# Performance work log

Measured on AMD Instinct MI355X. Metric: run time of the kernel, lower is better.

The kernel has to match this reference:

```python
import jax, jax.numpy as jnp
import numpy as np

B, N, FEAT = 64, 4096, 256
DIM, KVQ, HEADS, SLOTS, ITERS = 256, 256, 4, 8, 3
DPH = KVQ // HEADS
SCALE = DPH ** -0.5
EPS = 1e-8
LN_EPS = 1e-5


def layer_norm(x, w, b):
    mu = x.mean(-1, keepdims=True)
    var = ((x - mu) ** 2).mean(-1, keepdims=True)
    return (x - mu) * jax.lax.rsqrt(var + LN_EPS) * w + b


def setup_inputs() -> dict:
    key = jax.random.key(0)
    ks = jax.random.split(key, 12)
    s = 0.02
    return {
        "inputs": jax.random.normal(ks[0], (B, N, FEAT), jnp.float32),
        "conditioning": jax.random.normal(ks[1], (B, SLOTS, DIM), jnp.float32),
        "ln_in_w": jnp.ones((FEAT,), jnp.float32),
        "ln_in_b": jnp.zeros((FEAT,), jnp.float32),
        "ln_slot_w": jnp.ones((DIM,), jnp.float32),
        "ln_slot_b": jnp.zeros((DIM,), jnp.float32),
        "Wq": jax.random.normal(ks[2], (KVQ, DIM), jnp.float32) * s,
        "Wk": jax.random.normal(ks[3], (KVQ, FEAT), jnp.float32) * s,
        "Wv": jax.random.normal(ks[4], (KVQ, FEAT), jnp.float32) * s,
        "gru_wih": jax.random.normal(ks[5], (3 * DIM, KVQ), jnp.float32) * s,
        "gru_whh": jax.random.normal(ks[6], (3 * DIM, DIM), jnp.float32) * s,
        "gru_bih": jnp.zeros((3 * DIM,), jnp.float32),
        "gru_bhh": jnp.zeros((3 * DIM,), jnp.float32),
    }


def _gru_cell(x, h, wih, whh, bih, bhh):
    # torch.nn.GRUCell semantics; x:[M,KVQ], h:[M,DIM]
    gx = x @ wih.T + bih  # [M, 3*DIM]
    gh = h @ whh.T + bhh
    xr, xz, xn = jnp.split(gx, 3, axis=-1)
    hr, hz, hn = jnp.split(gh, 3, axis=-1)
    r = jax.nn.sigmoid(xr + hr)
    z = jax.nn.sigmoid(xz + hz)
    n = jnp.tanh(xn + r * hn)
    return (1.0 - z) * n + z * h


def reference(inputs, conditioning, ln_in_w, ln_in_b, ln_slot_w, ln_slot_b,
              Wq, Wk, Wv, gru_wih, gru_whh, gru_bih, gru_bhh):
    b, n, _ = inputs.shape
    x = layer_norm(inputs, ln_in_w, ln_in_b)
    k = (x @ Wk.T).reshape(b, n, HEADS, DPH)
    v = (x @ Wv.T).reshape(b, n, HEADS, DPH)

    slots = conditioning
    attn_list = []
    for _ in range(ITERS):
        slots_prev = slots
        sn = layer_norm(slots, ln_slot_w, ln_slot_b)
        q = (sn @ Wq.T).reshape(b, SLOTS, HEADS, DPH) * SCALE
        dots = jnp.einsum('bihd,bjhd->bihj', q, k)  # [b, SLOTS, HEADS, n]
        # softmax over flattened (slots, heads) axis per input position j
        attn = jax.nn.softmax(dots.reshape(b, SLOTS * HEADS, n), axis=1)
        attn = attn.reshape(b, SLOTS, HEADS, n)
        attn_before = attn
        attn = attn / (attn.sum(-1, keepdims=True) + EPS)
        updates = jnp.einsum('bjhd,bihj->bihd', v, attn).reshape(b, SLOTS, KVQ)
        h = _gru_cell(updates.reshape(-1, KVQ), slots_prev.reshape(-1, DIM),
                      gru_wih, gru_whh, gru_bih, gru_bhh)
        slots = h.reshape(b, SLOTS, DIM)
        attn_list.append(attn_before.mean(axis=2))  # [b, SLOTS, n]

    return slots, attn_list[-1], jnp.stack(attn_list)
```

## Files before the change

kernel.cpp:

```cpp
#include <hip/hip_runtime.h>
#include <hip/hip_bf16.h>


typedef unsigned int u32;
typedef unsigned short u16;
typedef short bf16x8 __attribute__((ext_vector_type(8)));
typedef float f32x4 __attribute__((ext_vector_type(4)));

#define SCALE_ 0.125f

__device__ inline u16 f2bf(float f){
  u32 x = __float_as_uint(f);
  return (u16)((x + 0x7fffu + ((x >> 16) & 1u)) >> 16);
}
__device__ inline float bf2f_s(short h){ return __uint_as_float(((u32)(u16)h) << 16); }

__device__ inline void gload16(const void* g, void* l){
  __builtin_amdgcn_global_load_lds((const __attribute__((address_space(1))) u32*)g,
                                   (__attribute__((address_space(3))) u32*)l, 16, 0, 0);
}

__global__ void prep_kernel(const float* __restrict__ Wk, const float* __restrict__ Wv,
                            const float* __restrict__ wih, const float* __restrict__ whh,
                            u16* __restrict__ Bkv, u16* __restrict__ wihb, u16* __restrict__ whhb){
  int t = blockIdx.x * 256 + threadIdx.x;
  int stride = gridDim.x * 256;
  for (int idx = t; idx < 512 * 256; idx += stride){
    int n = idx >> 8, c = idx & 255;
    float v = (n < 256) ? Wk[(n << 8) + c] : Wv[((n - 256) << 8) + c];
    Bkv[idx] = f2bf(v);
  }
  for (int idx = t; idx < 768 * 256; idx += stride){
    wihb[idx] = f2bf(wih[idx]);
    whhb[idx] = f2bf(whh[idx]);
  }
}

__global__ __launch_bounds__(256) void ln_in_kernel(const float* __restrict__ x,
    const float* __restrict__ w, const float* __restrict__ bb, u16* __restrict__ xn){
  int wid = threadIdx.x >> 6, lane = threadIdx.x & 63;
  long row = (long)blockIdx.x * 4 + wid;
  const float4* xr = (const float4*)(x + row * 256);
  float4 v = xr[lane];
  float s  = v.x + v.y + v.z + v.w;
  float s2 = v.x*v.x + v.y*v.y + v.z*v.z + v.w*v.w;
  #pragma unroll
  for (int m = 1; m < 64; m <<= 1){ s += __shfl_xor(s, m); s2 += __shfl_xor(s2, m); }
  float mu = s * (1.f/256.f);
  float rstd = rsqrtf(s2 * (1.f/256.f) - mu*mu + 1e-5f);
  float4 wv = ((const float4*)w)[lane];
  float4 bv = ((const float4*)bb)[lane];
  ushort4 o;
  o.x = f2bf((v.x - mu) * rstd * wv.x + bv.x);
  o.y = f2bf((v.y - mu) * rstd * wv.y + bv.y);
  o.z = f2bf((v.z - mu) * rstd * wv.z + bv.z);
  o.w = f2bf((v.w - mu) * rstd * wv.w + bv.w);
  *(ushort4*)(xn + row * 256 + lane * 4) = o;
}

__global__ __launch_bounds__(256) void gemm_kv(const u16* __restrict__ A,
                                               const u16* __restrict__ Bm,
                                               u16* __restrict__ kv){
  __shared__ u16 smem[16384];
  u16* Al = smem;
  u16* Bl = smem + 8192;
  int tid = threadIdx.x, wid = tid >> 6, lane = tid & 63;
  int nt = blockIdx.x & 3;
  long mt = blockIdx.x >> 2;
  long m0 = mt * 128;
  int n0 = nt * 128;
  f32x4 acc[4][4] = {};
  int msub = (wid & 1) * 64, nsub = (wid >> 1) * 64;
  for (int kt = 0; kt < 4; ++kt){
    const char* Ag = (const char*)(A + m0 * 256 + kt * 64);
    const char* Bg = (const char*)(Bm + (long)n0 * 256 + kt * 64);
    #pragma unroll
    for (int p = 0; p < 4; ++p){
      int r0 = wid * 32 + p * 8;
      gload16(Ag + (long)(r0 + (lane >> 3)) * 512 + (lane & 7) * 16, (char*)Al + r0 * 128);
      gload16(Bg + (long)(r0 + (lane >> 3)) * 512 + (lane & 7) * 16, (char*)Bl + r0 * 128);
    }
    __syncthreads();
    #pragma unroll
    for (int kk = 0; kk < 2; ++kk){
      bf16x8 af[4], bfr[4];
      #pragma unroll
      for (int mi = 0; mi < 4; ++mi)
        af[mi] = *(const bf16x8*)(Al + (msub + mi*16 + (lane & 15)) * 64 + kk * 32 + (lane >> 4) * 8);
      #pragma unroll
      for (int ni = 0; ni < 4; ++ni)
        bfr[ni] = *(const bf16x8*)(Bl + (nsub + ni*16 + (lane & 15)) * 64 + kk * 32 + (lane >> 4) * 8);
      #pragma unroll
      for (int mi = 0; mi < 4; ++mi)
        #pragma unroll
        for (int ni = 0; ni < 4; ++ni)
          acc[mi][ni] = __builtin_amdgcn_mfma_f32_16x16x32_bf16(af[mi], bfr[ni], acc[mi][ni], 0, 0, 0);
    }
    __syncthreads();
  }
  u16* Ct = smem;
  #pragma unroll
  for (int mi = 0; mi < 4; ++mi){
    #pragma unroll
    for (int ni = 0; ni < 4; ++ni){
      int col = nsub + ni*16 + (lane & 15);
      #pragma unroll
      for (int r = 0; r < 4; ++r){
        int rowm = msub + mi*16 + (lane >> 4) * 4 + r;
        Ct[rowm * 128 + col] = f2bf(acc[mi][ni][r]);
      }
    }
  }
  __syncthreads();
  #pragma unroll
  for (int p = 0; p < 8; ++p){
    int g = p * 256 + tid;
    int row = g >> 4, pw = g & 15;
    long m = m0 + row;
    int j = (int)(m & 4095);
    int lloc = pw ^ (j & 7);
    uint4 val = *(const uint4*)(Ct + row * 128 + lloc * 8);
    *(uint4*)((char*)kv + m * 1024 + n0 * 2 + pw * 16) = val;
  }
}

__global__ __launch_bounds__(256) void q_kernel(const float* __restrict__ ssrc,
    const float* __restrict__ lnw, const float* __restrict__ lnb,
    const float* __restrict__ Wq, float* __restrict__ qout){
  __shared__ float sn[256];
  __shared__ float red[8];
  int row = blockIdx.x, t = threadIdx.x;
  int wid = t >> 6, lane = t & 63;
  float x = ssrc[row * 256 + t];
  float s = x, s2 = x * x;
  #pragma unroll
  for (int m = 1; m < 64; m <<= 1){ s += __shfl_xor(s, m); s2 += __shfl_xor(s2, m); }
  if (lane == 0){ red[wid] = s; red[4 + wid] = s2; }
  __syncthreads();
  s  = red[0] + red[1] + red[2] + red[3];
  s2 = red[4] + red[5] + red[6] + red[7];
  float mu = s * (1.f/256.f);
  float rstd = rsqrtf(s2 * (1.f/256.f) - mu*mu + 1e-5f);
  sn[t] = (x - mu) * rstd * lnw[t] + lnb[t];
  __syncthreads();
  const float4* wr = (const float4*)(Wq + t * 256);
  float acc = 0.f;
  #pragma unroll 8
  for (int c = 0; c < 64; ++c){
    float4 wv = wr[c];
    acc += wv.x * sn[c*4] + wv.y * sn[c*4+1] + wv.z * sn[c*4+2] + wv.w * sn[c*4+3];
  }
  qout[row * 256 + t] = acc * SCALE_;
}

__global__ __launch_bounds__(256) void iter_kernel(
    const u16* __restrict__ kv, const float* __restrict__ qg,
    float* __restrict__ upd, float* __restrict__ asum,
    float* __restrict__ out_stack, float* __restrict__ out_last, int write_last){
  __shared__ u16 kvl[32 * 512];
  __shared__ float ql[2048];
  __shared__ float expl[1024];
  __shared__ float rtot[32];
  int tid = threadIdx.x, wid = tid >> 6, lane = tid & 63;
  int b = blockIdx.x >> 4;
  int blk = blockIdx.x & 15;

  {
    const char* qsrc = (const char*)(qg + b * 2048);
    #pragma unroll
    for (int p = 0; p < 2; ++p){
      int seg = wid * 2 + p;
      gload16(qsrc + seg * 1024 + lane * 16, (char*)ql + seg * 1024);
    }
  }
  float updacc[8];
  #pragma unroll
  for (int e = 0; e < 8; ++e) updacc[e] = 0.f;
  float asacc = 0.f;
  int i_u = tid >> 5, h_u = (tid >> 3) & 3, c_u = tid & 7;
  int jj = lane & 31, half = lane >> 5, h = wid;

  for (int tile = 0; tile < 8; ++tile){
    int j0 = (blk * 8 + tile) * 32;
    const char* src = (const char*)(kv + ((long)b * 4096 + j0) * 512);
    #pragma unroll
    for (int p = 0; p < 8; ++p){
      int seg = wid * 8 + p;
      gload16(src + seg * 1024 + lane * 16, (char*)kvl + seg * 1024);
    }
    __syncthreads();
    float dots[8];
    #pragma unroll
    for (int i = 0; i < 8; ++i) dots[i] = 0.f;
    #pragma unroll
    for (int cc = 0; cc < 4; ++cc){
      int c = half * 4 + cc;
      int gq = jj * 64 + ((h * 8 + c) ^ (jj & 7));
      bf16x8 kvv = *(const bf16x8*)(kvl + gq * 8);
      float kf[8];
      #pragma unroll
      for (int e = 0; e < 8; ++e) kf[e] = bf2f_s(kvv[e]);
      #pragma unroll
      for (int i = 0; i < 8; ++i){
        const float4* q4 = (const float4*)(ql + ((i * 4 + h) << 6) + c * 8);
        float4 qa = q4[0], qb = q4[1];
        dots[i] += qa.x*kf[0] + qa.y*kf[1] + qa.z*kf[2] + qa.w*kf[3]
                 + qb.x*kf[4] + qb.y*kf[5] + qb.z*kf[6] + qb.w*kf[7];
      }
    }
    #pragma unroll
    for (int i = 0; i < 8; ++i) dots[i] += __shfl_xor(dots[i], 32);
    float ev[8];
    #pragma unroll
    for (int i = 0; i < 8; ++i) ev[i] = __expf(dots[i]);
    #pragma unroll
    for (int r = 0; r < 4; ++r){
      int i = half * 4 + r;
      expl[jj * 32 + ((h * 8 + i) ^ jj)] = ev[i];
    }
    __syncthreads();
    if (wid == 0 && lane < 32){
      int j = lane;
      float tot = 0.f; float si[8];
      #pragma unroll
      for (int i = 0; i < 8; ++i) si[i] = 0.f;
      #pragma unroll
      for (int h2 = 0; h2 < 4; ++h2){
        #pragma unroll
        for (int i = 0; i < 8; ++i){
          float v = expl[j * 32 + ((h2 * 8 + i) ^ j)];
          tot += v; si[i] += v;
        }
      }
      float rt = 1.f / tot;
      rtot[j] = rt;
      long obase = ((long)b * 8) * 4096 + j0 + j;
      #pragma unroll
      for (int i = 0; i < 8; ++i){
        float o = 0.25f * si[i] * rt;
        out_stack[obase + (long)i * 4096] = o;
        if (write_last) out_last[obase + (long)i * 4096] = o;
      }
    }
    __syncthreads();
    #pragma unroll 4
    for (int j = 0; j < 32; ++j){
      float at = expl[j * 32 + ((h_u * 8 + i_u) ^ j)] * rtot[j];
      int gv = j * 64 + ((32 + h_u * 8 + c_u) ^ (j & 7));
      bf16x8 vv = *(const bf16x8*)(kvl + gv * 8);
      #pragma unroll
      for (int e = 0; e < 8; ++e) updacc[e] += at * bf2f_s(vv[e]);
      if (c_u == 0) asacc += at;
    }
    __syncthreads();
  }
  float* up = upd + (((long)b * 8 + i_u) << 8) + h_u * 64 + c_u * 8;
  #pragma unroll
  for (int e = 0; e < 8; ++e) atomicAdd(up + e, updacc[e]);
  if (c_u == 0) atomicAdd(asum + ((b * 8 + i_u) << 2) + h_u, asacc);
}

__global__ __launch_bounds__(256) void gru_kernel(const float* __restrict__ upd,
    const float* __restrict__ asum, const float* __restrict__ hsrc,
    const u16* __restrict__ wihb, const u16* __restrict__ whhb,
    const float* __restrict__ bih, const float* __restrict__ bhh,
    float* __restrict__ slots_ws, float* __restrict__ out_slots, int write_out){
  __shared__ float xs[256], hs[256];
  int row = blockIdx.x, t = threadIdx.x;
  float a = asum[(row << 2) + (t >> 6)];
  xs[t] = upd[(row << 8) + t] / (a + 1e-8f);
  hs[t] = hsrc[(row << 8) + t];
  __syncthreads();
  float gx[3], gh[3];
  #pragma unroll
  for (int g = 0; g < 3; ++g){
    const bf16x8* wr = (const bf16x8*)(wihb + (g * 256 + t) * 256);
    const bf16x8* wh = (const bf16x8*)(whhb + (g * 256 + t) * 256);
    float ax = 0.f, ah = 0.f;
    for (int c = 0; c < 32; ++c){
      bf16x8 w1 = wr[c], w2 = wh[c];
      #pragma unroll
      for (int e = 0; e < 8; ++e){
        ax += bf2f_s(w1[e]) * xs[c * 8 + e];
        ah += bf2f_s(w2[e]) * hs[c * 8 + e];
      }
    }
    gx[g] = ax + bih[g * 256 + t];
    gh[g] = ah + bhh[g * 256 + t];
  }
  float r = 1.f / (1.f + __expf(-(gx[0] + gh[0])));
  float z = 1.f / (1.f + __expf(-(gx[1] + gh[1])));
  float n = tanhf(gx[2] + r * gh[2]);
  float hnew = (1.f - z) * n + z * hs[t];
  slots_ws[(row << 8) + t] = hnew;
  if (write_out) out_slots[(row << 8) + t] = hnew;
}

extern "C" void kernel_launch(void* const* d_in, const int* in_sizes, int n_in,
                              void* d_out, int out_size, void* d_ws, size_t ws_size,
                              hipStream_t stream){
  const float* inputs = (const float*)d_in[0];
  const float* cond   = (const float*)d_in[1];
  const float* lniw   = (const float*)d_in[2];
  const float* lnib   = (const float*)d_in[3];
  const float* lnsw   = (const float*)d_in[4];
  const float* lnsb   = (const float*)d_in[5];
  const float* Wq     = (const float*)d_in[6];
  const float* Wk     = (const float*)d_in[7];
  const float* Wv     = (const float*)d_in[8];
  const float* wih    = (const float*)d_in[9];
  const float* whh    = (const float*)d_in[10];
  const float* bih    = (const float*)d_in[11];
  const float* bhh    = (const float*)d_in[12];

  char* ws = (char*)d_ws;
  u16*   xn       = (u16*)(ws);
  u16*   kv       = (u16*)(ws + 134217728);
  float* q_ws     = (float*)(ws + 402653184);
  float* slots_ws = (float*)(ws + 403177472);
  float* upd_ws   = (float*)(ws + 403701760);
  float* asum_ws  = (float*)(ws + 404226048);
  u16*   Bkv      = (u16*)(ws + 404234240);
  u16*   wihb     = (u16*)(ws + 404496384);
  u16*   whhb     = (u16*)(ws + 404889600);

  float* out       = (float*)d_out;
  float* out_slots = out;
  float* out_last  = out + 131072;
  float* out_stack = out + 131072 + 2097152;

  prep_kernel<<<dim3(256), dim3(256), 0, stream>>>(Wk, Wv, wih, whh, Bkv, wihb, whhb);
  ln_in_kernel<<<dim3(65536), dim3(256), 0, stream>>>(inputs, lniw, lnib, xn);
  gemm_kv<<<dim3(8192), dim3(256), 0, stream>>>(xn, Bkv, kv);
  for (int it = 0; it < 3; ++it){
    const float* ssrc = (it == 0) ? cond : slots_ws;
    q_kernel<<<dim3(512), dim3(256), 0, stream>>>(ssrc, lnsw, lnsb, Wq, q_ws);
    hipMemsetAsync(upd_ws, 0, 524288 + 8192, stream);
    iter_kernel<<<dim3(1024), dim3(256), 0, stream>>>(kv, q_ws, upd_ws, asum_ws,
        out_stack + (long)it * 2097152, out_last, (it == 2) ? 1 : 0);
    gru_kernel<<<dim3(512), dim3(256), 0, stream>>>(upd_ws, asum_ws, ssrc, wihb, whhb,
        bih, bhh, slots_ws, out_slots, (it == 2) ? 1 : 0);
  }
}
```

Baseline: 1.172 ms.

## Fuse next-iteration query projection and buffer zeroing into GRU; remap GEMM blocks per XCD

The GRU kernel now also zeroes the update and attention-sum accumulators and computes the LayerNorm plus Wq projection for the next iteration. This removes the per-iteration q_kernel launch and the hipMemsetAsync; only the first query projection keeps a standalone launch. Separately, the KV GEMM remaps block indices so the four N tiles of each M tile land on the same XCD, aiming to share A-tile reads in that XCD's L2. In exchange the GRU kernel does more work per block and needs extra shared memory and barriers.

New measurement: 1.158 ms. Within noise of the previous version (-1.2%).

```diff
diff --git a/kernel.cpp b/kernel.cpp
--- a/kernel.cpp
+++ b/kernel.cpp
@@ -65,8 +65,11 @@
   u16* Al = smem;
   u16* Bl = smem + 8192;
   int tid = threadIdx.x, wid = tid >> 6, lane = tid & 63;
-  int nt = blockIdx.x & 3;
-  long mt = blockIdx.x >> 2;
+  int id = blockIdx.x;
+  int xcd = id & 7;
+  int lid = id >> 3;
+  long mt = (long)xcd * 256 + (lid >> 2);
+  int nt = lid & 3;
   long m0 = mt * 128;
   int n0 = nt * 128;
   f32x4 acc[4][4] = {};
@@ -126,7 +129,8 @@
 
 __global__ __launch_bounds__(256) void q_kernel(const float* __restrict__ ssrc,
     const float* __restrict__ lnw, const float* __restrict__ lnb,
-    const float* __restrict__ Wq, float* __restrict__ qout){
+    const float* __restrict__ Wq, float* __restrict__ qout,
+    float* __restrict__ upd_z, float* __restrict__ asum_z){
   __shared__ float sn[256];
   __shared__ float red[8];
   int row = blockIdx.x, t = threadIdx.x;
@@ -151,6 +155,8 @@
     acc += wv.x * sn[c*4] + wv.y * sn[c*4+1] + wv.z * sn[c*4+2] + wv.w * sn[c*4+3];
   }
   qout[row * 256 + t] = acc * SCALE_;
+  upd_z[(row << 8) + t] = 0.f;
+  if (t < 4) asum_z[(row << 2) + t] = 0.f;
 }
 
 __global__ __launch_bounds__(256) void iter_kernel(
@@ -264,8 +270,12 @@
     const float* __restrict__ asum, const float* __restrict__ hsrc,
     const u16* __restrict__ wihb, const u16* __restrict__ whhb,
     const float* __restrict__ bih, const float* __restrict__ bhh,
-    float* __restrict__ slots_ws, float* __restrict__ out_slots, int write_out){
-  __shared__ float xs[256], hs[256];
+    const float* __restrict__ lnsw, const float* __restrict__ lnsb,
+    const float* __restrict__ Wq,
+    float* __restrict__ slots_ws, float* __restrict__ q_ws,
+    float* __restrict__ out_slots, float* __restrict__ upd_z,
+    float* __restrict__ asum_z, int flags){
+  __shared__ float xs[256], hs[256], sn[256], red[8];
   int row = blockIdx.x, t = threadIdx.x;
   float a = asum[(row << 2) + (t >> 6)];
   xs[t] = upd[(row << 8) + t] / (a + 1e-8f);
@@ -293,7 +303,33 @@
   float n = tanhf(gx[2] + r * gh[2]);
   float hnew = (1.f - z) * n + z * hs[t];
   slots_ws[(row << 8) + t] = hnew;
-  if (write_out) out_slots[(row << 8) + t] = hnew;
+  if (flags & 1) out_slots[(row << 8) + t] = hnew;
+  if (flags & 4){
+    upd_z[(row << 8) + t] = 0.f;
+    if (t < 4) asum_z[(row << 2) + t] = 0.f;
+  }
+  if (flags & 2){
+    int wid = t >> 6, lane = t & 63;
+    float s = hnew, s2 = hnew * hnew;
+    #pragma unroll
+    for (int m = 1; m < 64; m <<= 1){ s += __shfl_xor(s, m); s2 += __shfl_xor(s2, m); }
+    if (lane == 0){ red[wid] = s; red[4 + wid] = s2; }
+    __syncthreads();
+    s  = red[0] + red[1] + red[2] + red[3];
+    s2 = red[4] + red[5] + red[6] + red[7];
+    float mu = s * (1.f/256.f);
+    float rstd = rsqrtf(s2 * (1.f/256.f) - mu*mu + 1e-5f);
+    sn[t] = (hnew - mu) * rstd * lnsw[t] + lnsb[t];
+    __syncthreads();
+    const float4* wr = (const float4*)(Wq + t * 256);
+    float acc = 0.f;
+    #pragma unroll 8
+    for (int c = 0; c < 64; ++c){
+      float4 wv = wr[c];
+      acc += wv.x * sn[c*4] + wv.y * sn[c*4+1] + wv.z * sn[c*4+2] + wv.w * sn[c*4+3];
+    }
+    q_ws[(row << 8) + t] = acc * SCALE_;
+  }
 }
 
 extern "C" void kernel_launch(void* const* d_in, const int* in_sizes, int n_in,
@@ -332,13 +368,13 @@
   prep_kernel<<<dim3(256), dim3(256), 0, stream>>>(Wk, Wv, wih, whh, Bkv, wihb, whhb);
   ln_in_kernel<<<dim3(65536), dim3(256), 0, stream>>>(inputs, lniw, lnib, xn);
   gemm_kv<<<dim3(8192), dim3(256), 0, stream>>>(xn, Bkv, kv);
+  q_kernel<<<dim3(512), dim3(256), 0, stream>>>(cond, lnsw, lnsb, Wq, q_ws, upd_ws, asum_ws);
   for (int it = 0; it < 3; ++it){
     const float* ssrc = (it == 0) ? cond : slots_ws;
-    q_kernel<<<dim3(512), dim3(256), 0, stream>>>(ssrc, lnsw, lnsb, Wq, q_ws);
-    hipMemsetAsync(upd_ws, 0, 524288 + 8192, stream);
     iter_kernel<<<dim3(1024), dim3(256), 0, stream>>>(kv, q_ws, upd_ws, asum_ws,
         out_stack + (long)it * 2097152, out_last, (it == 2) ? 1 : 0);
+    int flags = (it == 2) ? 1 : (2 | 4);
     gru_kernel<<<dim3(512), dim3(256), 0, stream>>>(upd_ws, asum_ws, ssrc, wihb, whhb,
-        bih, bhh, slots_ws, out_slots, (it == 2) ? 1 : 0);
-  }
-}
+        bih, bhh, lnsw, lnsb, Wq, slots_ws, q_ws, out_slots, upd_ws, asum_ws, flags);
+  }
+}
```
